# Kernel tuning notes

Hardware: AMD Instinct MI355X
Metric: run time of the kernel (lower is better)

## Reference

```python
import jax, jax.numpy as jnp
import numpy as np

B, L, D, K, J = 8, 2048, 1024, 32, 512


def setup_inputs() -> dict:
    key = jax.random.key(0)
    ks = jax.random.split(key, 12)
    w = lambda k: jax.random.normal(k, (D, D), jnp.float32) * 0.02
    z = jnp.zeros((D,), jnp.float32)
    return {
        "seg0": jax.random.normal(ks[0], (B, L, D), jnp.float32),
        "seg1": jax.random.normal(ks[1], (B, L, D), jnp.float32),
        "prompt_embed": jax.random.normal(ks[2], (1, 1, D), jnp.float32),
        "Wq_mem": w(ks[3]), "bq_mem": z,
        "Wk_mem": w(ks[4]), "bk_mem": z,
        "Wq": w(ks[5]), "bq": z,
        "Wk": w(ks[6]), "bk": z,
        "Wv": w(ks[7]), "bv": z,
        "Wo": w(ks[8]), "bo": z,
    }


def reference(seg0, seg1, prompt_embed, Wq_mem, bq_mem, Wk_mem, bk_mem,
              Wq, bq, Wk, bk, Wv, bv, Wo, bo):
    scale = 1.0 / np.sqrt(D).astype(np.float32)  # n_heads=1 so d_k = d_model

    def backbone(X):  # single-head SDPA, X: [B, S, D]
        Q = X @ Wq + bq
        Kh = X @ Wk + bk
        V = X @ Wv + bv
        scores = jnp.einsum('bqd,bkd->bqk', Q, Kh) * scale
        attn = jax.nn.softmax(scores, axis=-1)
        out = jnp.einsum('bqk,bkd->bqd', attn, V)
        return out @ Wo + bo

    def summarize(H):  # -> [B, 1, D]
        T = jnp.broadcast_to(prompt_embed, (H.shape[0], 1, D))
        inp = jnp.concatenate([T, H[:, :J, :], T], axis=1)  # [B, J+2, D]
        return backbone(inp)[:, J:J + 1, :]

    # ---- segment 1: memory bank empty -> retrieval is zeros ----
    P0 = jnp.zeros((B, 1, D), seg0.dtype)
    input_h0 = jnp.concatenate([P0, seg0, P0], axis=1)  # [B, L+2, D]
    H_out0 = backbone(input_h0)[:, K + 1:L + K + 2, :]   # clamped slice -> [B, 2017, D]
    out0 = H_out0[:, :-1, :]                             # [B, 2016, D]
    M1 = H_out0[:, -1, :]                                # [B, D] stored memory
    prev_sensory = seg0[:, -K:, :]                       # [B, K, D]

    # ---- segment 2: soft retrieval over 1-entry memory bank ----
    S1 = summarize(seg1)                                 # [B, 1, D]
    M_past = M1[None]                                    # [1, B, D]
    Qn = S1 @ Wq_mem + bq_mem                            # [B, 1, D]
    Kp = M_past @ Wk_mem + bk_mem                        # [1, B, D]
    scores = jnp.matmul(Qn, jnp.swapaxes(Kp, -2, -1)) * scale  # [B, 1, B]
    attn = jax.nn.softmax(scores, axis=-1)
    P1 = jnp.matmul(attn, M_past)                        # [B, 1, D]

    input_h1 = jnp.concatenate([prev_sensory, P1, seg1, P1], axis=1)  # [B, K+L+2, D]
    H_out1 = backbone(input_h1)[:, K + 1:L + K + 2, :]   # [B, 2049, D]
    out1 = H_out1[:, :-1, :]                             # [B, 2048, D]
    return (out0, out1)
```

## Files before the change

kernel.cpp:

```cpp
#include <hip/hip_runtime.h>
#include <stdint.h>
#include <stddef.h>

#define DIM    1024
#define NBATCH 8
#define SEQL   2048
#define JSUM   512
#define SPMAX  2304

typedef unsigned long long ull;
typedef __attribute__((ext_vector_type(8))) __bf16 bf16x8;
typedef __attribute__((ext_vector_type(8))) short  short8;
typedef __attribute__((ext_vector_type(4))) float  floatx4;

__device__ __forceinline__ short f2bf(float f) {
  unsigned u = __builtin_bit_cast(unsigned, f);
  u = (u + 0x7fffu + ((u >> 16) & 1u)) >> 16;
  return (short)u;
}
__device__ __forceinline__ float bf2f(short s) {
  unsigned u = ((unsigned)(unsigned short)s) << 16;
  return __builtin_bit_cast(float, u);
}

__device__ __forceinline__ void glds16(const short* g, short8* l) {
  __builtin_amdgcn_global_load_lds(
      (const __attribute__((address_space(1))) unsigned int*)g,
      (__attribute__((address_space(3))) unsigned int*)l, 16, 0, 0);
}

#define VMCNT(n) do { asm volatile("s_waitcnt vmcnt(" #n ")" ::: "memory"); \
                      __builtin_amdgcn_sched_barrier(0); } while (0)

__device__ __forceinline__ void barrier_raw() {
  asm volatile("" ::: "memory");
  __builtin_amdgcn_s_barrier();
  asm volatile("" ::: "memory");
}

template<int MODE, int SWIZ>
__global__ __launch_bounds__(512, 2)
void gemm_nt(const short* __restrict__ A, ull sA, int ldA,
             const short* __restrict__ Bm, ull sB, int ldB,
             short* __restrict__ Cb, ull sC,
             int N, int Kd,
             const float* __restrict__ bias,
             float* __restrict__ dst0, int t_lo, int t_hi, int outT,
             float* __restrict__ dstSp, int t_sp, int Spad)
{
  int tn, tm, bz;
  if (SWIZ == 1) {
    const unsigned gx = gridDim.x;
    ull lin = blockIdx.x + (ull)gx * (blockIdx.y + (ull)gridDim.y * blockIdx.z);
    bz = (int)(lin & 7);
    ull s = lin >> 3;
    tn = (int)(s % gx);
    tm = (int)(s / gx);
  } else {
    tm = blockIdx.x; tn = blockIdx.y; bz = 0;
  }

  A  += (ull)bz * sA;
  Bm += (ull)bz * sB;

  const int tid  = threadIdx.x;
  const int wave = tid >> 6, lane = tid & 63;

  __shared__ short8 ldsA[2][2048];
  __shared__ short8 ldsB[2][2048];

  const int r0  = tid & 255;
  const int k80 = tid >> 8;
  const short* pA = A  + (long long)(tm * 256 + r0) * ldA + k80 * 8;
  const short* pB = Bm + (long long)(tn * 256 + r0) * ldB + k80 * 8;

  floatx4 acc[8][4];
#pragma unroll
  for (int i = 0; i < 8; i++)
#pragma unroll
    for (int j = 0; j < 4; j++) acc[i][j] = (floatx4)(0.0f);

  const int wm = (wave >> 2) * 128;
  const int wn = (wave & 3) * 64;
  const int fr = lane & 15;
  const int fq = lane >> 4;

  const int nt = Kd >> 6;

  glds16(pA,      &ldsA[0][tid]);
  glds16(pA + 16, &ldsA[0][tid + 512]);
  glds16(pB,      &ldsB[0][tid]);
  glds16(pB + 16, &ldsB[0][tid + 512]);
  glds16(pA + 32, &ldsA[0][1024 + tid]);
  glds16(pA + 48, &ldsA[0][1024 + tid + 512]);
  glds16(pB + 32, &ldsB[0][1024 + tid]);
  glds16(pB + 48, &ldsB[0][1024 + tid + 512]);
  VMCNT(4);
  barrier_raw();

  for (int t = 0; t < nt; t++) {
    const short8* LA = ldsA[t & 1];
    const short8* LB = ldsB[t & 1];
    const int  nb   = (t + 1) & 1;
    const int  koff = (t + 1) * 64;
    const bool stg  = (t + 1) < nt;

    bf16x8 af[4], bv[4];

    {
      const int ka = fq * 256;
#pragma unroll
      for (int mt = 0; mt < 4; mt++)
        af[mt] = __builtin_bit_cast(bf16x8, LA[ka + wm + mt * 16 + fr]);
#pragma unroll
      for (int n2 = 0; n2 < 4; n2++)
        bv[n2] = __builtin_bit_cast(bf16x8, LB[ka + wn + n2 * 16 + fr]);
      if (stg) {
        glds16(pA + koff,      &ldsA[nb][tid]);
        glds16(pA + koff + 16, &ldsA[nb][tid + 512]);
      }
      barrier_raw();
      __builtin_amdgcn_s_setprio(1);
#pragma unroll
      for (int mt = 0; mt < 4; mt++)
#pragma unroll
        for (int n2 = 0; n2 < 4; n2++)
          acc[mt][n2] = __builtin_amdgcn_mfma_f32_16x16x32_bf16(
              af[mt], bv[n2], acc[mt][n2], 0, 0, 0);
      __builtin_amdgcn_s_setprio(0);
      barrier_raw();
    }

    {
      const int ka = fq * 256;
#pragma unroll
      for (int mt = 0; mt < 4; mt++)
        af[mt] = __builtin_bit_cast(bf16x8, LA[ka + wm + 64 + mt * 16 + fr]);
      if (stg) {
        glds16(pB + koff,      &ldsB[nb][tid]);
        glds16(pB + koff + 16, &ldsB[nb][tid + 512]);
      }
      barrier_raw();
      __builtin_amdgcn_s_setprio(1);
#pragma unroll
      for (int mt = 0; mt < 4; mt++)
#pragma unroll
        for (int n2 = 0; n2 < 4; n2++)
          acc[4 + mt][n2] = __builtin_amdgcn_mfma_f32_16x16x32_bf16(
              af[mt], bv[n2], acc[4 + mt][n2], 0, 0, 0);
      __builtin_amdgcn_s_setprio(0);
      if (stg) VMCNT(4); else VMCNT(0);
      barrier_raw();
    }

    {
      const int ka = (fq + 4) * 256;
#pragma unroll
      for (int mt = 0; mt < 4; mt++)
        af[mt] = __builtin_bit_cast(bf16x8, LA[ka + wm + mt * 16 + fr]);
#pragma unroll
      for (int n2 = 0; n2 < 4; n2++)
        bv[n2] = __builtin_bit_cast(bf16x8, LB[ka + wn + n2 * 16 + fr]);
      if (stg) {
        glds16(pA + koff + 32, &ldsA[nb][1024 + tid]);
        glds16(pA + koff + 48, &ldsA[nb][1024 + tid + 512]);
      }
      barrier_raw();
      __builtin_amdgcn_s_setprio(1);
#pragma unroll
      for (int mt = 0; mt < 4; mt++)
#pragma unroll
        for (int n2 = 0; n2 < 4; n2++)
          acc[mt][n2] = __builtin_amdgcn_mfma_f32_16x16x32_bf16(
              af[mt], bv[n2], acc[mt][n2], 0, 0, 0);
      __builtin_amdgcn_s_setprio(0);
      barrier_raw();
    }

    {
      const int ka = (fq + 4) * 256;
#pragma unroll
      for (int mt = 0; mt < 4; mt++)
        af[mt] = __builtin_bit_cast(bf16x8, LA[ka + wm + 64 + mt * 16 + fr]);
      if (stg) {
        glds16(pB + koff + 32, &ldsB[nb][1024 + tid]);
        glds16(pB + koff + 48, &ldsB[nb][1024 + tid + 512]);
      }
      barrier_raw();
      __builtin_amdgcn_s_setprio(1);
#pragma unroll
      for (int mt = 0; mt < 4; mt++)
#pragma unroll
        for (int n2 = 0; n2 < 4; n2++)
          acc[4 + mt][n2] = __builtin_amdgcn_mfma_f32_16x16x32_bf16(
              af[mt], bv[n2], acc[4 + mt][n2], 0, 0, 0);
      __builtin_amdgcn_s_setprio(0);
      if (stg) VMCNT(4);
      barrier_raw();
    }
  }

  if (MODE == 3) {
    const int bb  = (tm * 256) / Spad;
    const int rb0 = tm * 256 - bb * Spad + wm + fq * 4;
#pragma unroll
    for (int mf = 0; mf < 8; mf++) {
#pragma unroll
      for (int n2 = 0; n2 < 4; n2++) {
        const int col = tn * 256 + wn + n2 * 16 + fr;
#pragma unroll
        for (int r = 0; r < 4; r++) {
          const int tt = rb0 + (mf >> 2) * 64 + (mf & 3) * 16 + r;
          float v = acc[mf][n2][r] + bias[col];
          if (tt >= t_lo && tt < t_hi)
            dst0[((size_t)bb * outT + (tt - t_lo)) * DIM + col] = v;
          else if (tt == t_sp)
            dstSp[(size_t)bb * DIM + col] = v;
        }
      }
    }
  } else {
    short* C = Cb + (ull)bz * sC;
#pragma unroll
    for (int mf = 0; mf < 8; mf++) {
#pragma unroll
      for (int n2 = 0; n2 < 4; n2++) {
        const int col = tn * 256 + wn + n2 * 16 + fr;
        float bn = (MODE == 1) ? bias[col] : 0.0f;
#pragma unroll
        for (int r = 0; r < 4; r++) {
          const int row = tm * 256 + wm + (mf >> 2) * 64 + (mf & 3) * 16 + fq * 4 + r;
          float v = acc[mf][n2][r] + bn;
          if (MODE == 2) v += bias[row];
          C[(size_t)row * N + col] = f2bf(v);
        }
      }
    }
  }
}

__global__ __launch_bounds__(256)
void softmax_rows(short* __restrict__ SA, int Spad, int S, float scale)
{
  __shared__ float buf[SPMAX];
  __shared__ float red[8];
  const int t = blockIdx.x, b = blockIdx.y;
  short* row = SA + ((size_t)b * Spad + t) * Spad;
  const int tid = threadIdx.x;
  const int nv = S >> 3;

  float mx = -1e30f;
  for (int g = tid; g < nv; g += 256) {
    short8 v = ((const short8*)row)[g];
#pragma unroll
    for (int j = 0; j < 8; j++) {
      float f = bf2f(v[j]) * scale;
      buf[g * 8 + j] = f;
      mx = fmaxf(mx, f);
    }
  }
  for (int i = (nv << 3) + tid; i < S; i += 256) {
    float f = bf2f(row[i]) * scale;
    buf[i] = f;
    mx = fmaxf(mx, f);
  }
  for (int off = 32; off; off >>= 1) mx = fmaxf(mx, __shfl_down(mx, off, 64));
  if ((tid & 63) == 0) red[tid >> 6] = mx;
  __syncthreads();
  if (tid == 0) {
    float m = red[0];
    for (int w = 1; w < 4; w++) m = fmaxf(m, red[w]);
    red[0] = m;
  }
  __syncthreads();
  mx = red[0];

  float sum = 0.f;
  for (int i = tid; i < S; i += 256) {
    float e = __expf(buf[i] - mx);
    buf[i] = e;
    sum += e;
  }
  for (int off = 32; off; off >>= 1) sum += __shfl_down(sum, off, 64);
  if ((tid & 63) == 0) red[4 + (tid >> 6)] = sum;
  __syncthreads();
  if (tid == 0) red[4] = 1.0f / (red[4] + red[5] + red[6] + red[7]);
  __syncthreads();
  const float rinv = red[4];

  for (int g = tid; g < nv; g += 256) {
    short8 o;
#pragma unroll
    for (int j = 0; j < 8; j++) o[j] = f2bf(buf[g * 8 + j] * rinv);
    ((short8*)row)[g] = o;
  }
  for (int i = (nv << 3) + tid; i < S; i += 256) row[i] = f2bf(buf[i] * rinv);
  for (int i = S + tid; i < Spad; i += 256) row[i] = 0;
}

__global__ __launch_bounds__(256)
void wtrans(const float* __restrict__ W, short* __restrict__ WT)
{
  __shared__ float tile[32][33];
  const int bn = blockIdx.x * 32, bk = blockIdx.y * 32;
  const int tx = threadIdx.x & 31, ty = threadIdx.x >> 5;
#pragma unroll
  for (int j = 0; j < 4; j++)
    tile[ty + j * 8][tx] = W[(size_t)(bk + ty + j * 8) * DIM + bn + tx];
  __syncthreads();
#pragma unroll
  for (int j = 0; j < 4; j++)
    WT[(size_t)(bn + ty + j * 8) * DIM + bk + tx] = f2bf(tile[tx][ty + j * 8]);
}

__global__ __launch_bounds__(256)
void bcat(const float* __restrict__ a, const float* __restrict__ b,
          float* __restrict__ o)
{
  const int i = blockIdx.x * 256 + threadIdx.x;
  o[i] = (i < DIM) ? a[i] : b[i - DIM];
}

__global__ __launch_bounds__(256)
void assemble0(const float* __restrict__ seg0, short* __restrict__ X)
{
  const int Spad = SPMAX;
  const int b = blockIdx.y;
  const size_t lin = ((size_t)blockIdx.x * 256 + threadIdx.x) * 4;
  const int t = (int)(lin >> 10), d = (int)(lin & 1023);
  float4 v = make_float4(0.f, 0.f, 0.f, 0.f);
  if (t >= 1 && t <= SEQL)
    v = *(const float4*)(seg0 + ((size_t)b * SEQL + (t - 1)) * DIM + d);
  union { short s[4]; ull u; } o;
  o.s[0] = f2bf(v.x); o.s[1] = f2bf(v.y); o.s[2] = f2bf(v.z); o.s[3] = f2bf(v.w);
  *(ull*)(X + (size_t)b * Spad * DIM + lin) = o.u;
}

__global__ __launch_bounds__(256)
void assembleS(const float* __restrict__ seg1, const float* __restrict__ prompt,
               short* __restrict__ X)
{
  const int Spad = 768;
  const int b = blockIdx.y;
  const size_t lin = ((size_t)blockIdx.x * 256 + threadIdx.x) * 4;
  const int t = (int)(lin >> 10), d = (int)(lin & 1023);
  float4 v = make_float4(0.f, 0.f, 0.f, 0.f);
  if (t == 0 || t == JSUM + 1)
    v = *(const float4*)(prompt + d);
  else if (t >= 1 && t <= JSUM)
    v = *(const float4*)(seg1 + ((size_t)b * SEQL + (t - 1)) * DIM + d);
  union { short s[4]; ull u; } o;
  o.s[0] = f2bf(v.x); o.s[1] = f2bf(v.y); o.s[2] = f2bf(v.z); o.s[3] = f2bf(v.w);
  *(ull*)(X + (size_t)b * Spad * DIM + lin) = o.u;
}

__global__ __launch_bounds__(256)
void assemble1(const float* __restrict__ seg0, const float* __restrict__ seg1,
               const float* __restrict__ P1, short* __restrict__ X)
{
  const int Spad = SPMAX;
  const int b = blockIdx.y;
  const size_t lin = ((size_t)blockIdx.x * 256 + threadIdx.x) * 4;
  const int t = (int)(lin >> 10), d = (int)(lin & 1023);
  float4 v = make_float4(0.f, 0.f, 0.f, 0.f);
  if (t < 32)
    v = *(const float4*)(seg0 + ((size_t)b * SEQL + (SEQL - 32 + t)) * DIM + d);
  else if (t == 32 || t == 2081)
    v = *(const float4*)(P1 + (size_t)b * DIM + d);
  else if (t >= 33 && t <= 2080)
    v = *(const float4*)(seg1 + ((size_t)b * SEQL + (t - 33)) * DIM + d);
  union { short s[4]; ull u; } o;
  o.s[0] = f2bf(v.x); o.s[1] = f2bf(v.y); o.s[2] = f2bf(v.z); o.s[3] = f2bf(v.w);
  *(ull*)(X + (size_t)b * Spad * DIM + lin) = o.u;
}

__global__ __launch_bounds__(256)
void mem_proj(const float* __restrict__ Sb, const float* __restrict__ M1,
              const float* __restrict__ Wq_mem, const float* __restrict__ bq_mem,
              const float* __restrict__ Wk_mem, const float* __restrict__ bk_mem,
              float* __restrict__ Qn, float* __restrict__ Kp)
{
  const int n = blockIdx.x * 256 + threadIdx.x;
  const int b = blockIdx.y;
  const int w = blockIdx.z;
  const float* x    = w ? M1 : Sb;
  const float* W    = w ? Wk_mem : Wq_mem;
  const float* bias = w ? bk_mem : bq_mem;
  float* o          = w ? Kp : Qn;
  const float* xr = x + (size_t)b * DIM;
  float s = bias[n];
  for (int k = 0; k < DIM; k++) s += xr[k] * W[(size_t)k * DIM + n];
  o[(size_t)b * DIM + n] = s;
}

__global__ __launch_bounds__(256)
void mem_attn(const float* __restrict__ Qn, const float* __restrict__ Kp,
              const float* __restrict__ M1, float* __restrict__ P1, float scale)
{
  __shared__ float red[256];
  __shared__ float w8[8];
  const int b = blockIdx.x, tid = threadIdx.x;
  for (int bp = 0; bp < NBATCH; bp++) {
    float p = 0.f;
    for (int k = tid; k < DIM; k += 256)
      p += Qn[(size_t)b * DIM + k] * Kp[(size_t)bp * DIM + k];
    red[tid] = p; __syncthreads();
    for (int off = 128; off; off >>= 1) {
      if (tid < off) red[tid] += red[tid + off];
      __syncthreads();
    }
    if (tid == 0) w8[bp] = red[0] * scale;
    __syncthreads();
  }
  if (tid == 0) {
    float m = w8[0];
    for (int i = 1; i < NBATCH; i++) m = fmaxf(m, w8[i]);
    float s = 0.f;
    for (int i = 0; i < NBATCH; i++) { w8[i] = __expf(w8[i] - m); s += w8[i]; }
    for (int i = 0; i < NBATCH; i++) w8[i] /= s;
  }
  __syncthreads();
  for (int d = tid; d < DIM; d += 256) {
    float a = 0.f;
    for (int bp = 0; bp < NBATCH; bp++) a += w8[bp] * M1[(size_t)bp * DIM + d];
    P1[(size_t)b * DIM + d] = a;
  }
}

extern "C" void kernel_launch(void* const* d_in, const int* in_sizes, int n_in,
                              void* d_out, int out_size, void* d_ws, size_t ws_size,
                              hipStream_t stream)
{
  const float* seg0   = (const float*)d_in[0];
  const float* seg1   = (const float*)d_in[1];
  const float* prompt = (const float*)d_in[2];
  const float* Wq_mem = (const float*)d_in[3];
  const float* bq_mem = (const float*)d_in[4];
  const float* Wk_mem = (const float*)d_in[5];
  const float* bk_mem = (const float*)d_in[6];
  const float* Wq     = (const float*)d_in[7];
  const float* bq     = (const float*)d_in[8];
  const float* Wk     = (const float*)d_in[9];
  const float* bk     = (const float*)d_in[10];
  const float* Wv     = (const float*)d_in[11];
  const float* bv     = (const float*)d_in[12];
  const float* Wo     = (const float*)d_in[13];
  const float* bo     = (const float*)d_in[14];
  float* outp = (float*)d_out;

  const size_t WSZ  = (size_t)DIM * DIM * 2;
  const size_t XSZ  = (size_t)NBATCH * SPMAX * DIM * 2;
  const size_t SASZ = (size_t)NBATCH * SPMAX * SPMAX * 2;
  const size_t VSZ  = (size_t)NBATCH * DIM * 4;

  char* p = (char*)d_ws;
  short* WqT = (short*)p; p += WSZ;
  short* WkT = (short*)p; p += WSZ;
  short* WvT = (short*)p; p += WSZ;
  short* WoT = (short*)p; p += WSZ;
  short* X   = (short*)p; p += XSZ;
  short* QKb = (short*)p; p += 2 * XSZ;
  short* Vt  = (short*)p; p += XSZ;
  short* Ctx = (short*)p; p += XSZ;
  short* SA  = (short*)p; p += SASZ;
  float* M1b = (float*)p; p += VSZ;
  float* Sb  = (float*)p; p += VSZ;
  float* Qn  = (float*)p; p += VSZ;
  float* Kp  = (float*)p; p += VSZ;
  float* P1  = (float*)p; p += VSZ;
  float* bqk = (float*)p; p += 2 * DIM * 4;

  const float scale = 0.03125f;
  dim3 blk(256, 1, 1);
  dim3 blkG(512, 1, 1);

  auto run_backbone = [&](int Spad, int S, int kAV,
                          float* o_dst, int t_lo, int t_hi, int outT,
                          float* o_sp, int t_sp) {
    const int MT = NBATCH * Spad / 256;
    gemm_nt<1, 2><<<dim3(MT, 2048 / 256, 1), blkG, 0, stream>>>(
        X, 0ULL, DIM, WqT, 0ULL, DIM, QKb, 0ULL, 2048, DIM, bqk,
        nullptr, 0, 0, 0, nullptr, -1, Spad);
    gemm_nt<2, 1><<<dim3(Spad / 256, DIM / 256, NBATCH), blkG, 0, stream>>>(
        WvT, 0ULL, DIM, X, (ull)Spad * DIM, DIM,
        Vt, (ull)DIM * Spad, Spad, DIM, bv,
        nullptr, 0, 0, 0, nullptr, -1, Spad);
    gemm_nt<0, 1><<<dim3(Spad / 256, Spad / 256, NBATCH), blkG, 0, stream>>>(
        QKb, (ull)Spad * 2048, 2048, QKb + DIM, (ull)Spad * 2048, 2048,
        SA, (ull)Spad * Spad, Spad, DIM, nullptr,
        nullptr, 0, 0, 0, nullptr, -1, Spad);
    softmax_rows<<<dim3(Spad, NBATCH), blk, 0, stream>>>(SA, Spad, S, scale);
    gemm_nt<0, 1><<<dim3(DIM / 256, Spad / 256, NBATCH), blkG, 0, stream>>>(
        SA, (ull)Spad * Spad, Spad, Vt, (ull)DIM * Spad, Spad,
        Ctx, (ull)Spad * DIM, DIM, kAV, nullptr,
        nullptr, 0, 0, 0, nullptr, -1, Spad);
    gemm_nt<3, 2><<<dim3(MT, DIM / 256, 1), blkG, 0, stream>>>(
        Ctx, 0ULL, DIM, WoT, 0ULL, DIM, nullptr, 0ULL, DIM, DIM, bo,
        o_dst, t_lo, t_hi, outT, o_sp, t_sp, Spad);
  };

  wtrans<<<dim3(32, 32), blk, 0, stream>>>(Wq, WqT);
  wtrans<<<dim3(32, 32), blk, 0, stream>>>(Wk, WkT);
  wtrans<<<dim3(32, 32), blk, 0, stream>>>(Wv, WvT);
  wtrans<<<dim3(32, 32), blk, 0, stream>>>(Wo, WoT);
  bcat<<<dim3(8), blk, 0, stream>>>(bq, bk, bqk);

  assemble0<<<dim3(SPMAX, NBATCH), blk, 0, stream>>>(seg0, X);
  run_backbone(SPMAX, 2050, 2112, outp, 33, 2049, 2016, M1b, 2049);

  assembleS<<<dim3(768, NBATCH), blk, 0, stream>>>(seg1, prompt, X);
  run_backbone(768, 514, 576, nullptr, 0, 0, 0, Sb, JSUM);

  mem_proj<<<dim3(DIM / 256, NBATCH, 2), blk, 0, stream>>>(
      Sb, M1b, Wq_mem, bq_mem, Wk_mem, bk_mem, Qn, Kp);
  mem_attn<<<dim3(NBATCH), blk, 0, stream>>>(Qn, Kp, M1b, P1, scale);

  assemble1<<<dim3(SPMAX, NBATCH), blk, 0, stream>>>(seg0, seg1, P1, X);
  run_backbone(SPMAX, 2082, 2112, outp + (size_t)NBATCH * 2016 * DIM,
               33, 2081, 2048, nullptr, -1);
}
```

Before: 1.552 ms.

## Batch segment-0 and summary backbones into shared grouped GEMM launches

Segment 0's backbone and the summary backbone are independent, so they now run together. Each GEMM stage and the softmax launch once with a flat grid covering both problems. A parameter struct lets each block pick its sub-problem by block index. The summary pass gets its own workspace buffers. This removes six kernel launches and fills the GPU better for the small summary GEMMs that would otherwise underuse it. The cost is more workspace memory and struct-based parameter indexing inside the kernel.

```diff
diff --git a/kernel.cpp b/kernel.cpp
--- a/kernel.cpp
+++ b/kernel.cpp
@@ -7,6 +7,7 @@
 #define SEQL   2048
 #define JSUM   512
 #define SPMAX  2304
+#define SPS    768
 
 typedef unsigned long long ull;
 typedef __attribute__((ext_vector_type(8))) __bf16 bf16x8;
@@ -38,30 +39,41 @@
   asm volatile("" ::: "memory");
 }
 
+struct GemmP {
+  const short* A; ull sA; int ldA;
+  const short* B; ull sB; int ldB;
+  short* C; ull sC;
+  int N, Kd;
+  const float* bias;
+  float* dst0; int t_lo, t_hi, outT;
+  float* dstSp; int t_sp, Spad;
+  int gx;
+  int nblk;
+};
+
 template<int MODE, int SWIZ>
 __global__ __launch_bounds__(512, 2)
-void gemm_nt(const short* __restrict__ A, ull sA, int ldA,
-             const short* __restrict__ Bm, ull sB, int ldB,
-             short* __restrict__ Cb, ull sC,
-             int N, int Kd,
-             const float* __restrict__ bias,
-             float* __restrict__ dst0, int t_lo, int t_hi, int outT,
-             float* __restrict__ dstSp, int t_sp, int Spad)
-{
+void gemm_nt(GemmP q0, GemmP q1)
+{
+  const int  pid = blockIdx.x;
+  const bool s1  = pid >= q0.nblk;
+  const GemmP& q = s1 ? q1 : q0;
+  const int  lid = s1 ? (pid - q0.nblk) : pid;
+
   int tn, tm, bz;
   if (SWIZ == 1) {
-    const unsigned gx = gridDim.x;
-    ull lin = blockIdx.x + (ull)gx * (blockIdx.y + (ull)gridDim.y * blockIdx.z);
-    bz = (int)(lin & 7);
-    ull s = lin >> 3;
-    tn = (int)(s % gx);
-    tm = (int)(s / gx);
+    bz = lid & 7;
+    const int s = lid >> 3;
+    tn = s % q.gx;
+    tm = s / q.gx;
   } else {
-    tm = blockIdx.x; tn = blockIdx.y; bz = 0;
-  }
-
-  A  += (ull)bz * sA;
-  Bm += (ull)bz * sB;
+    tm = lid % q.gx;
+    tn = lid / q.gx;
+    bz = 0;
+  }
+
+  const short* A  = q.A + (ull)bz * q.sA;
+  const short* Bm = q.B + (ull)bz * q.sB;
 
   const int tid  = threadIdx.x;
   const int wave = tid >> 6, lane = tid & 63;
@@ -71,8 +83,8 @@
 
   const int r0  = tid & 255;
   const int k80 = tid >> 8;
-  const short* pA = A  + (long long)(tm * 256 + r0) * ldA + k80 * 8;
-  const short* pB = Bm + (long long)(tn * 256 + r0) * ldB + k80 * 8;
+  const short* pA = A  + (long long)(tm * 256 + r0) * q.ldA + k80 * 8;
+  const short* pB = Bm + (long long)(tn * 256 + r0) * q.ldB + k80 * 8;
 
   floatx4 acc[8][4];
 #pragma unroll
@@ -85,7 +97,7 @@
   const int fr = lane & 15;
   const int fq = lane >> 4;
 
-  const int nt = Kd >> 6;
+  const int nt = q.Kd >> 6;
 
   glds16(pA,      &ldsA[0][tid]);
   glds16(pA + 16, &ldsA[0][tid + 512]);
@@ -201,8 +213,8 @@
   }
 
   if (MODE == 3) {
-    const int bb  = (tm * 256) / Spad;
-    const int rb0 = tm * 256 - bb * Spad + wm + fq * 4;
+    const int bb  = (tm * 256) / q.Spad;
+    const int rb0 = tm * 256 - bb * q.Spad + wm + fq * 4;
 #pragma unroll
     for (int mf = 0; mf < 8; mf++) {
 #pragma unroll
@@ -211,28 +223,28 @@
 #pragma unroll
         for (int r = 0; r < 4; r++) {
           const int tt = rb0 + (mf >> 2) * 64 + (mf & 3) * 16 + r;
-          float v = acc[mf][n2][r] + bias[col];
-          if (tt >= t_lo && tt < t_hi)
-            dst0[((size_t)bb * outT + (tt - t_lo)) * DIM + col] = v;
-          else if (tt == t_sp)
-            dstSp[(size_t)bb * DIM + col] = v;
+          float v = acc[mf][n2][r] + q.bias[col];
+          if (tt >= q.t_lo && tt < q.t_hi)
+            q.dst0[((size_t)bb * q.outT + (tt - q.t_lo)) * DIM + col] = v;
+          else if (tt == q.t_sp)
+            q.dstSp[(size_t)bb * DIM + col] = v;
         }
       }
     }
   } else {
-    short* C = Cb + (ull)bz * sC;
+    short* C = q.C + (ull)bz * q.sC;
 #pragma unroll
     for (int mf = 0; mf < 8; mf++) {
 #pragma unroll
       for (int n2 = 0; n2 < 4; n2++) {
         const int col = tn * 256 + wn + n2 * 16 + fr;
-        float bn = (MODE == 1) ? bias[col] : 0.0f;
+        float bn = (MODE == 1) ? q.bias[col] : 0.0f;
 #pragma unroll
         for (int r = 0; r < 4; r++) {
           const int row = tm * 256 + wm + (mf >> 2) * 64 + (mf & 3) * 16 + fq * 4 + r;
           float v = acc[mf][n2][r] + bn;
-          if (MODE == 2) v += bias[row];
-          C[(size_t)row * N + col] = f2bf(v);
+          if (MODE == 2) v += q.bias[row];
+          C[(size_t)row * q.N + col] = f2bf(v);
         }
       }
     }
@@ -240,12 +252,16 @@
 }
 
 __global__ __launch_bounds__(256)
-void softmax_rows(short* __restrict__ SA, int Spad, int S, float scale)
+void softmax_rows2(short* __restrict__ SA0, int Spad0, int S0, int nx0,
+                   short* __restrict__ SA1, int Spad1, int S1, float scale)
 {
   __shared__ float buf[SPMAX];
   __shared__ float red[8];
-  const int t = blockIdx.x, b = blockIdx.y;
-  short* row = SA + ((size_t)b * Spad + t) * Spad;
+  int t = blockIdx.x;
+  const int b = blockIdx.y;
+  short* row; int Spad, S;
+  if (t < nx0) { row = SA0 + ((size_t)b * Spad0 + t) * Spad0; Spad = Spad0; S = S0; }
+  else { t -= nx0; row = SA1 + ((size_t)b * Spad1 + t) * Spad1; Spad = Spad1; S = S1; }
   const int tid = threadIdx.x;
   const int nv = S >> 3;
 
@@ -340,7 +356,7 @@
 void assembleS(const float* __restrict__ seg1, const float* __restrict__ prompt,
                short* __restrict__ X)
 {
-  const int Spad = 768;
+  const int Spad = SPS;
   const int b = blockIdx.y;
   const size_t lin = ((size_t)blockIdx.x * 256 + threadIdx.x) * 4;
   const int t = (int)(lin >> 10), d = (int)(lin & 1023);
@@ -448,55 +464,47 @@
   const float* bo     = (const float*)d_in[14];
   float* outp = (float*)d_out;
 
-  const size_t WSZ  = (size_t)DIM * DIM * 2;
-  const size_t XSZ  = (size_t)NBATCH * SPMAX * DIM * 2;
-  const size_t SASZ = (size_t)NBATCH * SPMAX * SPMAX * 2;
-  const size_t VSZ  = (size_t)NBATCH * DIM * 4;
+  const size_t WSZ   = (size_t)DIM * DIM * 2;
+  const size_t XSZ   = (size_t)NBATCH * SPMAX * DIM * 2;
+  const size_t SASZ  = (size_t)NBATCH * SPMAX * SPMAX * 2;
+  const size_t XSZS  = (size_t)NBATCH * SPS * DIM * 2;
+  const size_t SASZS = (size_t)NBATCH * SPS * SPS * 2;
+  const size_t VSZ   = (size_t)NBATCH * DIM * 4;
 
   char* p = (char*)d_ws;
-  short* WqT = (short*)p; p += WSZ;
-  short* WkT = (short*)p; p += WSZ;
-  short* WvT = (short*)p; p += WSZ;
-  short* WoT = (short*)p; p += WSZ;
-  short* X   = (short*)p; p += XSZ;
-  short* QKb = (short*)p; p += 2 * XSZ;
-  short* Vt  = (short*)p; p += XSZ;
-  short* Ctx = (short*)p; p += XSZ;
-  short* SA  = (short*)p; p += SASZ;
-  float* M1b = (float*)p; p += VSZ;
-  float* Sb  = (float*)p; p += VSZ;
-  float* Qn  = (float*)p; p += VSZ;
-  float* Kp  = (float*)p; p += VSZ;
-  float* P1  = (float*)p; p += VSZ;
-  float* bqk = (float*)p; p += 2 * DIM * 4;
+  short* WqT  = (short*)p; p += WSZ;
+  short* WkT  = (short*)p; p += WSZ;
+  short* WvT  = (short*)p; p += WSZ;
+  short* WoT  = (short*)p; p += WSZ;
+  short* X    = (short*)p; p += XSZ;
+  short* QKb  = (short*)p; p += 2 * XSZ;
+  short* Vt   = (short*)p; p += XSZ;
+  short* Ctx  = (short*)p; p += XSZ;
+  short* SA   = (short*)p; p += SASZ;
+  short* XS   = (short*)p; p += XSZS;
+  short* QKbS = (short*)p; p += 2 * XSZS;
+  short* VtS  = (short*)p; p += XSZS;
+  short* CtxS = (short*)p; p += XSZS;
+  short* SAS  = (short*)p; p += SASZS;
+  float* M1b  = (float*)p; p += VSZ;
+  float* Sb   = (float*)p; p += VSZ;
+  float* Qn   = (float*)p; p += VSZ;
+  float* Kp   = (float*)p; p += VSZ;
+  float* P1   = (float*)p; p += VSZ;
+  float* bqk  = (float*)p; p += 2 * DIM * 4;
 
   const float scale = 0.03125f;
   dim3 blk(256, 1, 1);
   dim3 blkG(512, 1, 1);
 
-  auto run_backbone = [&](int Spad, int S, int kAV,
-                          float* o_dst, int t_lo, int t_hi, int outT,
-                          float* o_sp, int t_sp) {
-    const int MT = NBATCH * Spad / 256;
-    gemm_nt<1, 2><<<dim3(MT, 2048 / 256, 1), blkG, 0, stream>>>(
-        X, 0ULL, DIM, WqT, 0ULL, DIM, QKb, 0ULL, 2048, DIM, bqk,
-        nullptr, 0, 0, 0, nullptr, -1, Spad);
-    gemm_nt<2, 1><<<dim3(Spad / 256, DIM / 256, NBATCH), blkG, 0, stream>>>(
-        WvT, 0ULL, DIM, X, (ull)Spad * DIM, DIM,
-        Vt, (ull)DIM * Spad, Spad, DIM, bv,
-        nullptr, 0, 0, 0, nullptr, -1, Spad);
-    gemm_nt<0, 1><<<dim3(Spad / 256, Spad / 256, NBATCH), blkG, 0, stream>>>(
-        QKb, (ull)Spad * 2048, 2048, QKb + DIM, (ull)Spad * 2048, 2048,
-        SA, (ull)Spad * Spad, Spad, DIM, nullptr,
-        nullptr, 0, 0, 0, nullptr, -1, Spad);
-    softmax_rows<<<dim3(Spad, NBATCH), blk, 0, stream>>>(SA, Spad, S, scale);
-    gemm_nt<0, 1><<<dim3(DIM / 256, Spad / 256, NBATCH), blkG, 0, stream>>>(
-        SA, (ull)Spad * Spad, Spad, Vt, (ull)DIM * Spad, Spad,
-        Ctx, (ull)Spad * DIM, DIM, kAV, nullptr,
-        nullptr, 0, 0, 0, nullptr, -1, Spad);
-    gemm_nt<3, 2><<<dim3(MT, DIM / 256, 1), blkG, 0, stream>>>(
-        Ctx, 0ULL, DIM, WoT, 0ULL, DIM, nullptr, 0ULL, DIM, DIM, bo,
-        o_dst, t_lo, t_hi, outT, o_sp, t_sp, Spad);
+  auto P = [](const short* A, ull sA, int ldA,
+              const short* B, ull sB, int ldB,
+              short* C, ull sC, int N, int Kd, const float* bias,
+              float* dst0, int t_lo, int t_hi, int outT,
+              float* dstSp, int t_sp, int Spad, int gx, int nblk) {
+    GemmP q{A, sA, ldA, B, sB, ldB, C, sC, N, Kd, bias,
+            dst0, t_lo, t_hi, outT, dstSp, t_sp, Spad, gx, nblk};
+    return q;
   };
 
   wtrans<<<dim3(32, 32), blk, 0, stream>>>(Wq, WqT);
@@ -506,16 +514,86 @@
   bcat<<<dim3(8), blk, 0, stream>>>(bq, bk, bqk);
 
   assemble0<<<dim3(SPMAX, NBATCH), blk, 0, stream>>>(seg0, X);
-  run_backbone(SPMAX, 2050, 2112, outp, 33, 2049, 2016, M1b, 2049);
-
-  assembleS<<<dim3(768, NBATCH), blk, 0, stream>>>(seg1, prompt, X);
-  run_backbone(768, 514, 576, nullptr, 0, 0, 0, Sb, JSUM);
+  assembleS<<<dim3(SPS, NBATCH), blk, 0, stream>>>(seg1, prompt, XS);
+
+  {
+    GemmP a = P(X, 0, DIM, WqT, 0, DIM, QKb, 0, 2048, DIM, bqk,
+                nullptr, 0, 0, 0, nullptr, -1, SPMAX, NBATCH * SPMAX / 256, 576);
+    GemmP b = P(XS, 0, DIM, WqT, 0, DIM, QKbS, 0, 2048, DIM, bqk,
+                nullptr, 0, 0, 0, nullptr, -1, SPS, NBATCH * SPS / 256, 192);
+    gemm_nt<1, 2><<<dim3(768), blkG, 0, stream>>>(a, b);
+  }
+  {
+    GemmP a = P(WvT, 0, DIM, X, (ull)SPMAX * DIM, DIM,
+                Vt, (ull)DIM * SPMAX, SPMAX, DIM, bv,
+                nullptr, 0, 0, 0, nullptr, -1, SPMAX, SPMAX / 256, 288);
+    GemmP b = P(WvT, 0, DIM, XS, (ull)SPS * DIM, DIM,
+                VtS, (ull)DIM * SPS, SPS, DIM, bv,
+                nullptr, 0, 0, 0, nullptr, -1, SPS, SPS / 256, 96);
+    gemm_nt<2, 1><<<dim3(384), blkG, 0, stream>>>(a, b);
+  }
+  {
+    GemmP a = P(QKb, (ull)SPMAX * 2048, 2048, QKb + DIM, (ull)SPMAX * 2048, 2048,
+                SA, (ull)SPMAX * SPMAX, SPMAX, DIM, nullptr,
+                nullptr, 0, 0, 0, nullptr, -1, SPMAX, SPMAX / 256, 648);
+    GemmP b = P(QKbS, (ull)SPS * 2048, 2048, QKbS + DIM, (ull)SPS * 2048, 2048,
+                SAS, (ull)SPS * SPS, SPS, DIM, nullptr,
+                nullptr, 0, 0, 0, nullptr, -1, SPS, SPS / 256, 72);
+    gemm_nt<0, 1><<<dim3(720), blkG, 0, stream>>>(a, b);
+  }
+  softmax_rows2<<<dim3(SPMAX + SPS, NBATCH), blk, 0, stream>>>(
+      SA, SPMAX, 2050, SPMAX, SAS, SPS, 514, scale);
+  {
+    GemmP a = P(SA, (ull)SPMAX * SPMAX, SPMAX, Vt, (ull)DIM * SPMAX, SPMAX,
+                Ctx, (ull)SPMAX * DIM, DIM, 2112, nullptr,
+                nullptr, 0, 0, 0, nullptr, -1, SPMAX, DIM / 256, 288);
+    GemmP b = P(SAS, (ull)SPS * SPS, SPS, VtS, (ull)DIM * SPS, SPS,
+                CtxS, (ull)SPS * DIM, DIM, 576, nullptr,
+                nullptr, 0, 0, 0, nullptr, -1, SPS, DIM / 256, 96);
+    gemm_nt<0, 1><<<dim3(384), blkG, 0, stream>>>(a, b);
+  }
+  {
+    GemmP a = P(Ctx, 0, DIM, WoT, 0, DIM, nullptr, 0, DIM, DIM, bo,
+                outp, 33, 2049, 2016, M1b, 2049, SPMAX, NBATCH * SPMAX / 256, 288);
+    GemmP b = P(CtxS, 0, DIM, WoT, 0, DIM, nullptr, 0, DIM, DIM, bo,
+                nullptr, 0, 0, 0, Sb, JSUM, SPS, NBATCH * SPS / 256, 96);
+    gemm_nt<3, 2><<<dim3(384), blkG, 0, stream>>>(a, b);
+  }
 
   mem_proj<<<dim3(DIM / 256, NBATCH, 2), blk, 0, stream>>>(
       Sb, M1b, Wq_mem, bq_mem, Wk_mem, bk_mem, Qn, Kp);
   mem_attn<<<dim3(NBATCH), blk, 0, stream>>>(Qn, Kp, M1b, P1, scale);
 
   assemble1<<<dim3(SPMAX, NBATCH), blk, 0, stream>>>(seg0, seg1, P1, X);
-  run_backbone(SPMAX, 2082, 2112, outp + (size_t)NBATCH * 2016 * DIM,
-               33, 2081, 2048, nullptr, -1);
-}
+  {
+    GemmP a = P(X, 0, DIM, WqT, 0, DIM, QKb, 0, 2048, DIM, bqk,
+                nullptr, 0, 0, 0, nullptr, -1, SPMAX, NBATCH * SPMAX / 256, 576);
+    gemm_nt<1, 2><<<dim3(576), blkG, 0, stream>>>(a, a);
+  }
+  {
+    GemmP a = P(WvT, 0, DIM, X, (ull)SPMAX * DIM, DIM,
+                Vt, (ull)DIM * SPMAX, SPMAX, DIM, bv,
+                nullptr, 0, 0, 0, nullptr, -1, SPMAX, SPMAX / 256, 288);
+    gemm_nt<2, 1><<<dim3(288), blkG, 0, stream>>>(a, a);
+  }
+  {
+    GemmP a = P(QKb, (ull)SPMAX * 2048, 2048, QKb + DIM, (ull)SPMAX * 2048, 2048,
+                SA, (ull)SPMAX * SPMAX, SPMAX, DIM, nullptr,
+                nullptr, 0, 0, 0, nullptr, -1, SPMAX, SPMAX / 256, 648);
+    gemm_nt<0, 1><<<dim3(648), blkG, 0, stream>>>(a, a);
+  }
+  softmax_rows2<<<dim3(SPMAX, NBATCH), blk, 0, stream>>>(
+      SA, SPMAX, 2082, SPMAX, SA, SPMAX, 2082, scale);
+  {
+    GemmP a = P(SA, (ull)SPMAX * SPMAX, SPMAX, Vt, (ull)DIM * SPMAX, SPMAX,
+                Ctx, (ull)SPMAX * DIM, DIM, 2112, nullptr,
+                nullptr, 0, 0, 0, nullptr, -1, SPMAX, DIM / 256, 288);
+    gemm_nt<0, 1><<<dim3(288), blkG, 0, stream>>>(a, a);
+  }
+  {
+    GemmP a = P(Ctx, 0, DIM, WoT, 0, DIM, nullptr, 0, DIM, DIM, bo,
+                outp + (size_t)NBATCH * 2016 * DIM, 33, 2081, 2048,
+                nullptr, -1, SPMAX, NBATCH * SPMAX / 256, 288);
+    gemm_nt<3, 2><<<dim3(288), blkG, 0, stream>>>(a, a);
+  }
+}
```

Result: faster. 1.442 ms (-7.1%).
